# Performance work log

Hardware: AMD Instinct MI355X
Metric: run time of the kernel (lower is better)

## Reference

```python
import jax, jax.numpy as jnp
import numpy as np

B, S, D, H, O = 128, 512, 128, 1024, 64
IN = 2 * D + 1  # input_size*2 + 1


def _xavier(key, shape):
    fan_out, fan_in = shape
    std = np.sqrt(2.0 / (fan_in + fan_out)).astype(np.float32)
    return jax.random.normal(key, shape, jnp.float32) * std


def setup_inputs() -> dict:
    key = jax.random.key(0)
    ks = jax.random.split(key, 6)
    x = jax.random.normal(ks[0], (B, S, D), jnp.float32)
    mask = jax.random.uniform(ks[1], (B, S, D), jnp.float32)
    ti = jax.random.uniform(ks[2], (B, S, 1), jnp.float32)
    W_ih = _xavier(ks[3], (4 * H, IN))   # LSTMCell weight_ih
    W_hh = _xavier(ks[4], (4 * H, H))    # LSTMCell weight_hh
    b_ih = jnp.zeros((4 * H,), jnp.float32)
    b_hh = jnp.zeros((4 * H,), jnp.float32)
    W_fc = _xavier(ks[5], (O, H))
    b_fc = jnp.zeros((O,), jnp.float32)
    return {"x": x, "mask": mask, "ti": ti, "W_ih": W_ih, "W_hh": W_hh,
            "b_ih": b_ih, "b_hh": b_hh, "W_fc": W_fc, "b_fc": b_fc}


def reference(x, mask, ti, W_ih, W_hh, b_ih, b_hh, W_fc, b_fc):
    b, s, _ = x.shape
    h = W_hh.shape[1]
    xt = jnp.concatenate([x, mask, ti], axis=-1)          # [B,S,IN]
    # Precompute input contribution to gates for all timesteps (one big GEMM)
    xg = jnp.einsum('bsi,gi->sbg', xt, W_ih) + b_ih + b_hh  # [S,B,4H]

    def step(carry, xg_t):
        h_t, c_t = carry
        g = xg_t + h_t @ W_hh.T                             # [B,4H]
        i, f, gg, o = jnp.split(g, 4, axis=-1)              # torch gate order i,f,g,o
        i = jax.nn.sigmoid(i)
        f = jax.nn.sigmoid(f)
        gg = jnp.tanh(gg)
        o = jax.nn.sigmoid(o)
        c_new = f * c_t + i * gg
        h_new = o * jnp.tanh(c_new)
        return (h_new, c_new), None

    h0 = jnp.zeros((b, h), x.dtype)
    c0 = jnp.zeros((b, h), x.dtype)
    (h_last, _), _ = jax.lax.scan(step, (h0, c0), xg)
    return h_last @ W_fc.T + b_fc                           # [B,O]
```

## Files before the change

### kernel.cpp

```cpp
#include <hip/hip_runtime.h>
#include <hip/hip_bf16.h>

typedef __bf16 bf16x8 __attribute__((ext_vector_type(8)));
typedef float f32x4 __attribute__((ext_vector_type(4)));
typedef unsigned int u32x4 __attribute__((ext_vector_type(4)));

#define BB   128
#define SS   512
#define DD   128
#define HH   1024
#define OO   64
#define IIN  257

#define NGROUP 2
#define GBLK   128
#define MG     64
#define NC     32
#define KK_H   32
#define KK_X   9

#define XTP_SLAB  18432
#define HBUF_SLAB 65536

#define WS_HBUF  1024
#define WS_HLAST 525312
#define WS_XTP   1049600

__device__ __forceinline__ u32x4 ldg_dev16(const void* p) {
  u32x4 r;
  asm volatile("global_load_dwordx4 %0, %1, off sc1" : "=v"(r) : "v"(p));
  return r;
}
__device__ __forceinline__ void stg_dev4(void* p, unsigned int v) {
  asm volatile("global_store_dword %0, %1, off sc1" :: "v"(p), "v"(v));
}
__device__ __forceinline__ bf16x8 asbf(u32x4 v) {
  union { u32x4 u; bf16x8 h; } c; c.u = v; return c.h;
}

#define CLAIMW(CNTSTR, A)                                            \
  asm volatile("s_waitcnt vmcnt(" CNTSTR ")"                         \
    : "+v"((A)[0]), "+v"((A)[1]), "+v"((A)[2]), "+v"((A)[3]),        \
      "+v"((A)[4]), "+v"((A)[5]), "+v"((A)[6]), "+v"((A)[7]))

__global__ void prepack_kernel(const float* __restrict__ x, const float* __restrict__ mask,
                               const float* __restrict__ ti, __bf16* __restrict__ xtp) {
  int idx = blockIdx.x * 256 + threadIdx.x;
  int slab = idx / XTP_SLAB;
  int rem  = idx - slab * XTP_SLAB;
  int p = slab & 1, t = slab >> 1;
  int j = rem & 7, l = (rem >> 3) & 63;
  int t2 = rem >> 9;
  int kk = t2 % 9, mt = t2 / 9;
  int b = p * MG + mt * 16 + (l & 15);
  int k = kk * 32 + ((l >> 4) << 3) + j;
  float v;
  if (k < 128)       v = x[(b * SS + t) * DD + k];
  else if (k < 256)  v = mask[(b * SS + t) * DD + (k - 128)];
  else if (k == 256) v = ti[b * SS + t];
  else               v = 0.f;
  xtp[idx] = (__bf16)v;
}

__device__ __forceinline__ float sigmoid_f(float v) { return 1.f / (1.f + __expf(-v)); }
__device__ __forceinline__ float tanh_f(float v)    { return 1.f - 2.f / (__expf(2.f * v) + 1.f); }

__launch_bounds__(256, 1)
__global__ void lstm_scan(const float* __restrict__ W_ih, const float* __restrict__ W_hh,
                          const float* __restrict__ b_ih, const float* __restrict__ b_hh,
                          const __bf16* __restrict__ xtp, __bf16* __restrict__ hbuf,
                          float* __restrict__ hlast, unsigned int* __restrict__ flags) {
  __shared__ __bf16 whh_lds[2 * KK_H * 512];
  __shared__ __bf16 wih_lds[2 * KK_X * 512];
  __shared__ float  bias_lds[NC];
  __shared__ float  gstage[64 * 36];
  __shared__ float  c_lds[512];

  const int tid = threadIdx.x;
  const int bid = blockIdx.x;
  const int r8  = bid & 7;
  const int p   = r8 >> 2;
  const int bIG = (bid >> 3) * 4 + (r8 & 3);
  const int j0  = bIG * 8;

  for (int e = tid; e < 2 * KK_H * 512; e += 256) {
    int j = e & 7, l = (e >> 3) & 63, kk = (e >> 9) & 31, nt = e >> 14;
    int n = nt * 16 + (l & 15);
    int col = ((n >> 3) << 10) + j0 + (n & 7);
    int k = kk * 32 + ((l >> 4) << 3) + j;
    whh_lds[e] = (__bf16)W_hh[col * HH + k];
  }
  for (int e = tid; e < 2 * KK_X * 512; e += 256) {
    int j = e & 7, l = (e >> 3) & 63;
    int t2 = e >> 9;
    int kk = t2 % 9, nt = t2 / 9;
    int n = nt * 16 + (l & 15);
    int col = ((n >> 3) << 10) + j0 + (n & 7);
    int k = kk * 32 + ((l >> 4) << 3) + j;
    wih_lds[e] = (k < IIN) ? (__bf16)W_ih[col * IIN + k] : (__bf16)0.f;
  }
  if (tid < NC) {
    int n = tid;
    int col = ((n >> 3) << 10) + j0 + (n & 7);
    bias_lds[n] = b_ih[col] + b_hh[col];
  }
  for (int e = tid; e < 512; e += 256) c_lds[e] = 0.f;
  __syncthreads();

  const int w = tid >> 6;
  const int l = tid & 63;
  unsigned int* gflags = flags + p * 128;

  for (int t = 0; t < SS; ++t) {
    const int rb = t & 1, wb = rb ^ 1;
    const __bf16* hb  = hbuf + (p * 2 + rb) * HBUF_SLAB + w * (KK_H * 512);
    const __bf16* xb  = xtp + (size_t)(t * 2 + p) * XTP_SLAB + w * (KK_X * 512);
    f32x4 acc0 = {0.f, 0.f, 0.f, 0.f};
    f32x4 acc1 = {0.f, 0.f, 0.f, 0.f};

    #pragma unroll
    for (int kk = 0; kk < KK_X; ++kk) {
      bf16x8 a  = *(const bf16x8*)(xb + kk * 512 + l * 8);
      bf16x8 b0 = *(const bf16x8*)(wih_lds + kk * 512 + l * 8);
      bf16x8 b1 = *(const bf16x8*)(wih_lds + KK_X * 512 + kk * 512 + l * 8);
      acc0 = __builtin_amdgcn_mfma_f32_16x16x32_bf16(a, b0, acc0, 0, 0, 0);
      acc1 = __builtin_amdgcn_mfma_f32_16x16x32_bf16(a, b1, acc1, 0, 0, 0);
    }

    if (t > 0) {
      if (tid < 64) {
        const unsigned int tgt = (unsigned int)t;
        for (;;) {
          unsigned int fa, fb;
          asm volatile("global_load_dword %0, %2, off sc1\n\t"
                       "global_load_dword %1, %3, off sc1\n\t"
                       "s_waitcnt vmcnt(0)"
                       : "=&v"(fa), "=&v"(fb)
                       : "v"(gflags + tid), "v"(gflags + 64 + tid));
          if (!__ballot(fa < tgt || fb < tgt)) break;
          __builtin_amdgcn_s_sleep(1);
        }
      }
      __syncthreads();
    }

    {
      const __bf16* hbL = hb + l * 8;
      u32x4 A0[8], A1[8];
      #pragma unroll
      for (int i = 0; i < 8; ++i) A0[i] = ldg_dev16(hbL + i * 512);
      #pragma unroll
      for (int i = 0; i < 8; ++i) A1[i] = ldg_dev16(hbL + (8 + i) * 512);

      CLAIMW("8", A0);
      #pragma unroll
      for (int i = 0; i < 8; ++i) {
        bf16x8 b0 = *(const bf16x8*)(whh_lds + i * 512 + l * 8);
        bf16x8 b1 = *(const bf16x8*)(whh_lds + KK_H * 512 + i * 512 + l * 8);
        acc0 = __builtin_amdgcn_mfma_f32_16x16x32_bf16(asbf(A0[i]), b0, acc0, 0, 0, 0);
        acc1 = __builtin_amdgcn_mfma_f32_16x16x32_bf16(asbf(A0[i]), b1, acc1, 0, 0, 0);
      }
      #pragma unroll
      for (int i = 0; i < 8; ++i) A0[i] = ldg_dev16(hbL + (16 + i) * 512);

      CLAIMW("8", A1);
      #pragma unroll
      for (int i = 0; i < 8; ++i) {
        int kk = 8 + i;
        bf16x8 b0 = *(const bf16x8*)(whh_lds + kk * 512 + l * 8);
        bf16x8 b1 = *(const bf16x8*)(whh_lds + KK_H * 512 + kk * 512 + l * 8);
        acc0 = __builtin_amdgcn_mfma_f32_16x16x32_bf16(asbf(A1[i]), b0, acc0, 0, 0, 0);
        acc1 = __builtin_amdgcn_mfma_f32_16x16x32_bf16(asbf(A1[i]), b1, acc1, 0, 0, 0);
      }
      #pragma unroll
      for (int i = 0; i < 8; ++i) A1[i] = ldg_dev16(hbL + (24 + i) * 512);

      CLAIMW("8", A0);
      #pragma unroll
      for (int i = 0; i < 8; ++i) {
        int kk = 16 + i;
        bf16x8 b0 = *(const bf16x8*)(whh_lds + kk * 512 + l * 8);
        bf16x8 b1 = *(const bf16x8*)(whh_lds + KK_H * 512 + kk * 512 + l * 8);
        acc0 = __builtin_amdgcn_mfma_f32_16x16x32_bf16(asbf(A0[i]), b0, acc0, 0, 0, 0);
        acc1 = __builtin_amdgcn_mfma_f32_16x16x32_bf16(asbf(A0[i]), b1, acc1, 0, 0, 0);
      }

      CLAIMW("0", A1);
      #pragma unroll
      for (int i = 0; i < 8; ++i) {
        int kk = 24 + i;
        bf16x8 b0 = *(const bf16x8*)(whh_lds + kk * 512 + l * 8);
        bf16x8 b1 = *(const bf16x8*)(whh_lds + KK_H * 512 + kk * 512 + l * 8);
        acc0 = __builtin_amdgcn_mfma_f32_16x16x32_bf16(asbf(A1[i]), b0, acc0, 0, 0, 0);
        acc1 = __builtin_amdgcn_mfma_f32_16x16x32_bf16(asbf(A1[i]), b1, acc1, 0, 0, 0);
      }
    }

    {
      int q = l >> 4, n = l & 15;
      float bi0 = bias_lds[n], bi1 = bias_lds[16 + n];
      #pragma unroll
      for (int rr = 0; rr < 4; ++rr) {
        int m = w * 16 + q * 4 + rr;
        gstage[m * 36 + n]      = acc0[rr] + bi0;
        gstage[m * 36 + 16 + n] = acc1[rr] + bi1;
      }
    }
    __syncthreads();

    {
      __bf16* hw = hbuf + (p * 2 + wb) * HBUF_SLAB;
      int m = tid >> 2, jq = tid & 3;
      int jb = 2 * jq;
      float h2[2];
      #pragma unroll
      for (int s = 0; s < 2; ++s) {
        int j = jb + s;
        float gi = gstage[m * 36 + j];
        float gf = gstage[m * 36 + 8 + j];
        float gg = gstage[m * 36 + 16 + j];
        float go = gstage[m * 36 + 24 + j];
        float i_ = sigmoid_f(gi);
        float f_ = sigmoid_f(gf);
        float g_ = tanh_f(gg);
        float o_ = sigmoid_f(go);
        float c  = f_ * c_lds[m * 8 + j] + i_ * g_;
        c_lds[m * 8 + j] = c;
        h2[s] = o_ * tanh_f(c);
      }
      union { __bf16 h[2]; unsigned int u; } pk;
      pk.h[0] = (__bf16)h2[0];
      pk.h[1] = (__bf16)h2[1];
      int k = j0 + jb;
      int mt = m >> 4, nn = m & 15, kk2 = k >> 5, q2 = (k >> 3) & 3;
      int off = ((mt * 32 + kk2) * 64 + q2 * 16 + nn) * 8 + jb;
      stg_dev4(hw + off, pk.u);
      if (t == SS - 1) {
        hlast[(p * MG + m) * HH + k]     = h2[0];
        hlast[(p * MG + m) * HH + k + 1] = h2[1];
      }
    }

    asm volatile("s_waitcnt vmcnt(0)" ::: "memory");
    __syncthreads();
    if (t < SS - 1 && tid == 0) {
      stg_dev4(gflags + bIG, (unsigned int)(t + 1));
    }
  }
}

__global__ void fc_kernel(const float* __restrict__ hlast, const float* __restrict__ W_fc,
                          const float* __restrict__ b_fc, float* __restrict__ out) {
  int b = blockIdx.x;
  int t = threadIdx.x;
  int o = t >> 2, part = t & 3;
  const float* hr = hlast + b * HH;
  const float* wr = W_fc + o * HH;
  float s = 0.f;
  #pragma unroll 4
  for (int k0 = part * 4; k0 < HH; k0 += 16) {
    float4 hv = *(const float4*)(hr + k0);
    float4 wv = *(const float4*)(wr + k0);
    s += hv.x * wv.x + hv.y * wv.y + hv.z * wv.z + hv.w * wv.w;
  }
  s += __shfl_xor(s, 1);
  s += __shfl_xor(s, 2);
  if (part == 0) out[b * OO + o] = s + b_fc[o];
}

extern "C" void kernel_launch(void* const* d_in, const int* in_sizes, int n_in,
                              void* d_out, int out_size, void* d_ws, size_t ws_size,
                              hipStream_t stream) {
  const float* x    = (const float*)d_in[0];
  const float* mask = (const float*)d_in[1];
  const float* ti   = (const float*)d_in[2];
  const float* W_ih = (const float*)d_in[3];
  const float* W_hh = (const float*)d_in[4];
  const float* b_ih = (const float*)d_in[5];
  const float* b_hh = (const float*)d_in[6];
  const float* W_fc = (const float*)d_in[7];
  const float* b_fc = (const float*)d_in[8];
  float* out = (float*)d_out;

  char* ws = (char*)d_ws;
  unsigned int* flags = (unsigned int*)ws;
  __bf16* hbuf  = (__bf16*)(ws + WS_HBUF);
  float*  hlast = (float*)(ws + WS_HLAST);
  __bf16* xtp   = (__bf16*)(ws + WS_XTP);

  hipMemsetAsync(ws, 0, WS_HLAST, stream);

  prepack_kernel<<<(1024 * XTP_SLAB) / 256, 256, 0, stream>>>(x, mask, ti, xtp);
  lstm_scan<<<NGROUP * GBLK, 256, 0, stream>>>(W_ih, W_hh, b_ih, b_hh, xtp, hbuf, hlast, flags);
  fc_kernel<<<BB, 256, 0, stream>>>(hlast, W_fc, b_fc, out);
}
```

Measured before the change: 2.422 ms.

## Halve scan blocks, widen hidden tile per block, stream W_ih from prepacked global

```diff
diff --git a/kernel.cpp b/kernel.cpp
--- a/kernel.cpp
+++ b/kernel.cpp
@@ -4,6 +4,7 @@
 typedef __bf16 bf16x8 __attribute__((ext_vector_type(8)));
 typedef float f32x4 __attribute__((ext_vector_type(4)));
 typedef unsigned int u32x4 __attribute__((ext_vector_type(4)));
+typedef unsigned int u32x2 __attribute__((ext_vector_type(2)));
 
 #define BB   128
 #define SS   512
@@ -13,18 +14,21 @@
 #define IIN  257
 
 #define NGROUP 2
-#define GBLK   128
+#define GBLK   64
 #define MG     64
-#define NC     32
+#define NC     64
+#define NT     4
 #define KK_H   32
 #define KK_X   9
 
 #define XTP_SLAB  18432
 #define HBUF_SLAB 65536
+#define WIH_BLK   (NT*KK_X*512)
 
 #define WS_HBUF  1024
 #define WS_HLAST 525312
 #define WS_XTP   1049600
+#define WS_WIHP  38798336
 
 __device__ __forceinline__ u32x4 ldg_dev16(const void* p) {
   u32x4 r;
@@ -33,6 +37,9 @@
 }
 __device__ __forceinline__ void stg_dev4(void* p, unsigned int v) {
   asm volatile("global_store_dword %0, %1, off sc1" :: "v"(p), "v"(v));
+}
+__device__ __forceinline__ void stg_dev8(void* p, u32x2 v) {
+  asm volatile("global_store_dwordx2 %0, %1, off sc1" :: "v"(p), "v"(v));
 }
 __device__ __forceinline__ bf16x8 asbf(u32x4 v) {
   union { u32x4 u; bf16x8 h; } c; c.u = v; return c.h;
@@ -62,82 +69,82 @@
   xtp[idx] = (__bf16)v;
 }
 
+__global__ void wih_prepack(const float* __restrict__ W_ih, __bf16* __restrict__ wihp) {
+  int idx = blockIdx.x * 256 + threadIdx.x;
+  int j = idx & 7, l = (idx >> 3) & 63;
+  int r = idx >> 9;
+  int kk = r % 9; int r2 = r / 9;
+  int nt = r2 & 3, blk = r2 >> 2;
+  int col = nt * HH + blk * 16 + (l & 15);
+  int k = kk * 32 + ((l >> 4) << 3) + j;
+  wihp[idx] = (k < IIN) ? (__bf16)W_ih[col * IIN + k] : (__bf16)0.f;
+}
+
 __device__ __forceinline__ float sigmoid_f(float v) { return 1.f / (1.f + __expf(-v)); }
 __device__ __forceinline__ float tanh_f(float v)    { return 1.f - 2.f / (__expf(2.f * v) + 1.f); }
 
 __launch_bounds__(256, 1)
-__global__ void lstm_scan(const float* __restrict__ W_ih, const float* __restrict__ W_hh,
+__global__ void lstm_scan(const float* __restrict__ W_hh,
                           const float* __restrict__ b_ih, const float* __restrict__ b_hh,
-                          const __bf16* __restrict__ xtp, __bf16* __restrict__ hbuf,
+                          const __bf16* __restrict__ xtp, const __bf16* __restrict__ wihp,
+                          __bf16* __restrict__ hbuf,
                           float* __restrict__ hlast, unsigned int* __restrict__ flags) {
-  __shared__ __bf16 whh_lds[2 * KK_H * 512];
-  __shared__ __bf16 wih_lds[2 * KK_X * 512];
+  __shared__ __bf16 whh_lds[NT * KK_H * 512];
+  __shared__ float  gstage[64 * 69];
   __shared__ float  bias_lds[NC];
-  __shared__ float  gstage[64 * 36];
-  __shared__ float  c_lds[512];
 
   const int tid = threadIdx.x;
   const int bid = blockIdx.x;
   const int r8  = bid & 7;
   const int p   = r8 >> 2;
   const int bIG = (bid >> 3) * 4 + (r8 & 3);
-  const int j0  = bIG * 8;
-
-  for (int e = tid; e < 2 * KK_H * 512; e += 256) {
+  const int j0  = bIG * 16;
+
+  for (int e = tid; e < NT * KK_H * 512; e += 256) {
     int j = e & 7, l = (e >> 3) & 63, kk = (e >> 9) & 31, nt = e >> 14;
-    int n = nt * 16 + (l & 15);
-    int col = ((n >> 3) << 10) + j0 + (n & 7);
+    int col = nt * HH + j0 + (l & 15);
     int k = kk * 32 + ((l >> 4) << 3) + j;
     whh_lds[e] = (__bf16)W_hh[col * HH + k];
   }
-  for (int e = tid; e < 2 * KK_X * 512; e += 256) {
-    int j = e & 7, l = (e >> 3) & 63;
-    int t2 = e >> 9;
-    int kk = t2 % 9, nt = t2 / 9;
-    int n = nt * 16 + (l & 15);
-    int col = ((n >> 3) << 10) + j0 + (n & 7);
-    int k = kk * 32 + ((l >> 4) << 3) + j;
-    wih_lds[e] = (k < IIN) ? (__bf16)W_ih[col * IIN + k] : (__bf16)0.f;
+  if (tid < NC) {
+    int col = (tid >> 4) * HH + j0 + (tid & 15);
+    bias_lds[tid] = b_ih[col] + b_hh[col];
   }
-  if (tid < NC) {
-    int n = tid;
-    int col = ((n >> 3) << 10) + j0 + (n & 7);
-    bias_lds[n] = b_ih[col] + b_hh[col];
-  }
-  for (int e = tid; e < 512; e += 256) c_lds[e] = 0.f;
   __syncthreads();
 
   const int w = tid >> 6;
   const int l = tid & 63;
   unsigned int* gflags = flags + p * 128;
+  const __bf16* wp = wihp + bIG * WIH_BLK;
+
+  float creg[4] = {0.f, 0.f, 0.f, 0.f};
 
   for (int t = 0; t < SS; ++t) {
     const int rb = t & 1, wb = rb ^ 1;
-    const __bf16* hb  = hbuf + (p * 2 + rb) * HBUF_SLAB + w * (KK_H * 512);
-    const __bf16* xb  = xtp + (size_t)(t * 2 + p) * XTP_SLAB + w * (KK_X * 512);
-    f32x4 acc0 = {0.f, 0.f, 0.f, 0.f};
-    f32x4 acc1 = {0.f, 0.f, 0.f, 0.f};
+    const __bf16* xb = xtp + (size_t)(t * 2 + p) * XTP_SLAB + w * (KK_X * 512);
+    f32x4 acc[NT];
+    #pragma unroll
+    for (int nt = 0; nt < NT; ++nt) acc[nt] = (f32x4){0.f, 0.f, 0.f, 0.f};
 
     #pragma unroll
     for (int kk = 0; kk < KK_X; ++kk) {
-      bf16x8 a  = *(const bf16x8*)(xb + kk * 512 + l * 8);
-      bf16x8 b0 = *(const bf16x8*)(wih_lds + kk * 512 + l * 8);
-      bf16x8 b1 = *(const bf16x8*)(wih_lds + KK_X * 512 + kk * 512 + l * 8);
-      acc0 = __builtin_amdgcn_mfma_f32_16x16x32_bf16(a, b0, acc0, 0, 0, 0);
-      acc1 = __builtin_amdgcn_mfma_f32_16x16x32_bf16(a, b1, acc1, 0, 0, 0);
+      bf16x8 a = *(const bf16x8*)(xb + kk * 512 + l * 8);
+      #pragma unroll
+      for (int nt = 0; nt < NT; ++nt) {
+        bf16x8 b = *(const bf16x8*)(wp + (nt * KK_X + kk) * 512 + l * 8);
+        acc[nt] = __builtin_amdgcn_mfma_f32_16x16x32_bf16(a, b, acc[nt], 0, 0, 0);
+      }
     }
 
     if (t > 0) {
       if (tid < 64) {
         const unsigned int tgt = (unsigned int)t;
         for (;;) {
-          unsigned int fa, fb;
-          asm volatile("global_load_dword %0, %2, off sc1\n\t"
-                       "global_load_dword %1, %3, off sc1\n\t"
+          unsigned int fa;
+          asm volatile("global_load_dword %0, %1, off sc1\n\t"
                        "s_waitcnt vmcnt(0)"
-                       : "=&v"(fa), "=&v"(fb)
-                       : "v"(gflags + tid), "v"(gflags + 64 + tid));
-          if (!__ballot(fa < tgt || fb < tgt)) break;
+                       : "=v"(fa) : "v"(gflags + tid));
+          if (!__ballot(fa < tgt)) break;
           __builtin_amdgcn_s_sleep(1);
         }
       }
@@ -145,7 +152,7 @@
     }
 
     {
-      const __bf16* hbL = hb + l * 8;
+      const __bf16* hbL = hbuf + (p * 2 + rb) * HBUF_SLAB + w * (KK_H * 512) + l * 8;
       u32x4 A0[8], A1[8];
       #pragma unroll
       for (int i = 0; i < 8; ++i) A0[i] = ldg_dev16(hbL + i * 512);
@@ -155,10 +162,11 @@
       CLAIMW("8", A0);
       #pragma unroll
       for (int i = 0; i < 8; ++i) {
-        bf16x8 b0 = *(const bf16x8*)(whh_lds + i * 512 + l * 8);
-        bf16x8 b1 = *(const bf16x8*)(whh_lds + KK_H * 512 + i * 512 + l * 8);
-        acc0 = __builtin_amdgcn_mfma_f32_16x16x32_bf16(asbf(A0[i]), b0, acc0, 0, 0, 0);
-        acc1 = __builtin_amdgcn_mfma_f32_16x16x32_bf16(asbf(A0[i]), b1, acc1, 0, 0, 0);
+        #pragma unroll
+        for (int nt = 0; nt < NT; ++nt) {
+          bf16x8 b = *(const bf16x8*)(whh_lds + (nt * KK_H + i) * 512 + l * 8);
+          acc[nt] = __builtin_amdgcn_mfma_f32_16x16x32_bf16(asbf(A0[i]), b, acc[nt], 0, 0, 0);
+        }
       }
       #pragma unroll
       for (int i = 0; i < 8; ++i) A0[i] = ldg_dev16(hbL + (16 + i) * 512);
@@ -167,10 +175,11 @@
       #pragma unroll
       for (int i = 0; i < 8; ++i) {
         int kk = 8 + i;
-        bf16x8 b0 = *(const bf16x8*)(whh_lds + kk * 512 + l * 8);
-        bf16x8 b1 = *(const bf16x8*)(whh_lds + KK_H * 512 + kk * 512 + l * 8);
-        acc0 = __builtin_amdgcn_mfma_f32_16x16x32_bf16(asbf(A1[i]), b0, acc0, 0, 0, 0);
-        acc1 = __builtin_amdgcn_mfma_f32_16x16x32_bf16(asbf(A1[i]), b1, acc1, 0, 0, 0);
+        #pragma unroll
+        for (int nt = 0; nt < NT; ++nt) {
+          bf16x8 b = *(const bf16x8*)(whh_lds + (nt * KK_H + kk) * 512 + l * 8);
+          acc[nt] = __builtin_amdgcn_mfma_f32_16x16x32_bf16(asbf(A1[i]), b, acc[nt], 0, 0, 0);
+        }
       }
       #pragma unroll
       for (int i = 0; i < 8; ++i) A1[i] = ldg_dev16(hbL + (24 + i) * 512);
@@ -179,65 +188,67 @@
       #pragma unroll
       for (int i = 0; i < 8; ++i) {
         int kk = 16 + i;
-        bf16x8 b0 = *(const bf16x8*)(whh_lds + kk * 512 + l * 8);
-        bf16x8 b1 = *(const bf16x8*)(whh_lds + KK_H * 512 + kk * 512 + l * 8);
-        acc0 = __builtin_amdgcn_mfma_f32_16x16x32_bf16(asbf(A0[i]), b0, acc0, 0, 0, 0);
-        acc1 = __builtin_amdgcn_mfma_f32_16x16x32_bf16(asbf(A0[i]), b1, acc1, 0, 0, 0);
+        #pragma unroll
+        for (int nt = 0; nt < NT; ++nt) {
+          bf16x8 b = *(const bf16x8*)(whh_lds + (nt * KK_H + kk) * 512 + l * 8);
+          acc[nt] = __builtin_amdgcn_mfma_f32_16x16x32_bf16(asbf(A0[i]), b, acc[nt], 0, 0, 0);
+        }
       }
 
       CLAIMW("0", A1);
       #pragma unroll
       for (int i = 0; i < 8; ++i) {
         int kk = 24 + i;
-        bf16x8 b0 = *(const bf16x8*)(whh_lds + kk * 512 + l * 8);
-        bf16x8 b1 = *(const bf16x8*)(whh_lds + KK_H * 512 + kk * 512 + l * 8);
-        acc0 = __builtin_amdgcn_mfma_f32_16x16x32_bf16(asbf(A1[i]), b0, acc0, 0, 0, 0);
-        acc1 = __builtin_amdgcn_mfma_f32_16x16x32_bf16(asbf(A1[i]), b1, acc1, 0, 0, 0);
+        #pragma unroll
+        for (int nt = 0; nt < NT; ++nt) {
+          bf16x8 b = *(const bf16x8*)(whh_lds + (nt * KK_H + kk) * 512 + l * 8);
+          acc[nt] = __builtin_amdgcn_mfma_f32_16x16x32_bf16(asbf(A1[i]), b, acc[nt], 0, 0, 0);
+        }
       }
     }
 
     {
-      int q = l >> 4, n = l & 15;
-      float bi0 = bias_lds[n], bi1 = bias_lds[16 + n];
-      #pragma unroll
-      for (int rr = 0; rr < 4; ++rr) {
-        int m = w * 16 + q * 4 + rr;
-        gstage[m * 36 + n]      = acc0[rr] + bi0;
-        gstage[m * 36 + 16 + n] = acc1[rr] + bi1;
-      }
-    }
-    __syncthreads();
+      int q = l >> 4, n16 = l & 15;
+      #pragma unroll
+      for (int nt = 0; nt < NT; ++nt) {
+        float bi = bias_lds[nt * 16 + n16];
+        #pragma unroll
+        for (int rr = 0; rr < 4; ++rr) {
+          int m = w * 16 + q * 4 + rr;
+          gstage[m * 69 + nt * 16 + n16] = acc[nt][rr] + bi;
+        }
+      }
+    }
+    asm volatile("s_waitcnt lgkmcnt(0)" ::: "memory");
 
     {
       __bf16* hw = hbuf + (p * 2 + wb) * HBUF_SLAB;
-      int m = tid >> 2, jq = tid & 3;
-      int jb = 2 * jq;
-      float h2[2];
-      #pragma unroll
-      for (int s = 0; s < 2; ++s) {
-        int j = jb + s;
-        float gi = gstage[m * 36 + j];
-        float gf = gstage[m * 36 + 8 + j];
-        float gg = gstage[m * 36 + 16 + j];
-        float go = gstage[m * 36 + 24 + j];
+      int mloc = l >> 2, m = w * 16 + mloc, jq = l & 3;
+      float h4[4];
+      #pragma unroll
+      for (int s = 0; s < 4; ++s) {
+        int jj = jq * 4 + s;
+        float gi = gstage[m * 69 + jj];
+        float gf = gstage[m * 69 + 16 + jj];
+        float gg = gstage[m * 69 + 32 + jj];
+        float go = gstage[m * 69 + 48 + jj];
         float i_ = sigmoid_f(gi);
         float f_ = sigmoid_f(gf);
         float g_ = tanh_f(gg);
         float o_ = sigmoid_f(go);
-        float c  = f_ * c_lds[m * 8 + j] + i_ * g_;
-        c_lds[m * 8 + j] = c;
-        h2[s] = o_ * tanh_f(c);
-      }
-      union { __bf16 h[2]; unsigned int u; } pk;
-      pk.h[0] = (__bf16)h2[0];
-      pk.h[1] = (__bf16)h2[1];
-      int k = j0 + jb;
-      int mt = m >> 4, nn = m & 15, kk2 = k >> 5, q2 = (k >> 3) & 3;
-      int off = ((mt * 32 + kk2) * 64 + q2 * 16 + nn) * 8 + jb;
-      stg_dev4(hw + off, pk.u);
+        float c  = f_ * creg[s] + i_ * g_;
+        creg[s] = c;
+        h4[s] = o_ * tanh_f(c);
+      }
+      union { __bf16 h[4]; u32x2 u; } pk;
+      #pragma unroll
+      for (int s = 0; s < 4; ++s) pk.h[s] = (__bf16)h4[s];
+      int k0 = j0 + jq * 4;
+      int off0 = ((w * 32 + (k0 >> 5)) * 64 + ((k0 >> 3) & 3) * 16 + mloc) * 8 + (k0 & 7);
+      stg_dev8(hw + off0, pk.u);
       if (t == SS - 1) {
-        hlast[(p * MG + m) * HH + k]     = h2[0];
-        hlast[(p * MG + m) * HH + k + 1] = h2[1];
+        f32x4 hv = {h4[0], h4[1], h4[2], h4[3]};
+        *(f32x4*)(hlast + (p * MG + m) * HH + k0) = hv;
       }
     }
 
@@ -287,10 +298,12 @@
   __bf16* hbuf  = (__bf16*)(ws + WS_HBUF);
   float*  hlast = (float*)(ws + WS_HLAST);
   __bf16* xtp   = (__bf16*)(ws + WS_XTP);
+  __bf16* wihp  = (__bf16*)(ws + WS_WIHP);
 
   hipMemsetAsync(ws, 0, WS_HLAST, stream);
 
   prepack_kernel<<<(1024 * XTP_SLAB) / 256, 256, 0, stream>>>(x, mask, ti, xtp);
-  lstm_scan<<<NGROUP * GBLK, 256, 0, stream>>>(W_ih, W_hh, b_ih, b_hh, xtp, hbuf, hlast, flags);
+  wih_prepack<<<(128 * WIH_BLK) / 256, 256, 0, stream>>>(W_ih, wihp);
+  lstm_scan<<<NGROUP * GBLK, 256, 0, stream>>>(W_hh, b_ih, b_hh, xtp, wihp, hbuf, hlast, flags);
   fc_kernel<<<BB, 256, 0, stream>>>(hlast, W_fc, b_fc, out);
 }
```

Result: slower. 3.951 ms (+63.2%).
